# Performance work log

Hardware: AMD Instinct MI355X
Metric: run time of the kernel (lower is better)

Reference implementation:

```python
import jax, jax.numpy as jnp
import numpy as np
from jax import lax

# 4 directional difference kernels, stacked as OIHW [4,1,3,3]
# torch conv2d is cross-correlation; lax.conv_general_dilated with OIHW/NCHW matches.
_KERNELS = jnp.array([
    [[0, 0, 0], [-1, 1, 0], [0, 0, 0]],   # left:  x[i,j] - x[i,j-1]
    [[0, 0, 0], [0, 1, -1], [0, 0, 0]],   # right: x[i,j] - x[i,j+1]
    [[0, -1, 0], [0, 1, 0], [0, 0, 0]],   # up:    x[i,j] - x[i-1,j]
    [[0, 0, 0], [0, 1, 0], [0, -1, 0]],   # down:  x[i,j] - x[i+1,j]
], dtype=jnp.float32)[:, None, :, :]


def _avg_pool4(x):
    # x: [B,1,H,W] -> [B,1,H//4,W//4], non-overlapping 4x4 mean
    B, C, H, W = x.shape
    return x.reshape(B, C, H // 4, 4, W // 4, 4).mean(axis=(3, 5))


def _dir_diffs(x):
    # x: [B,1,h,w] -> [B,4,h,w]; zero-padded cross-correlation, padding=1
    return lax.conv_general_dilated(
        x, _KERNELS, window_strides=(1, 1), padding=((1, 1), (1, 1)),
        dimension_numbers=("NCHW", "OIHW", "NCHW"))


def setup_inputs() -> dict:
    key = jax.random.key(0)
    k1, k2 = jax.random.split(key)
    original = jax.random.uniform(k1, (32, 3, 512, 512), dtype=jnp.float32)
    enhanced = jax.random.uniform(k2, (32, 3, 512, 512), dtype=jnp.float32)
    return {"original": original, "enhanced": enhanced}


def reference(original, enhanced) -> jnp.ndarray:
    # channel mean, keepdim -> [B,1,H,W]
    o = jnp.mean(original, axis=1, keepdims=True)
    e = jnp.mean(enhanced, axis=1, keepdims=True)
    # 4x4 avg pool -> [B,1,H/4,W/4]
    op = _avg_pool4(o)
    ep = _avg_pool4(e)
    # 4 directional shift-diffs for both, squared differences summed over directions
    d = _dir_diffs(op) - _dir_diffs(ep)           # [B,4,h,w]
    loss = jnp.sum(d * d, axis=1, keepdims=True)  # [B,1,h,w]
    return loss
```

## Files before the change

### kernel.cpp

```cpp
#include <hip/hip_runtime.h>

#define HH 512
#define WW 512
#define PH 128
#define PW 128
#define CC 3

typedef float f32x4 __attribute__((ext_vector_type(4)));

__global__ void __launch_bounds__(256, 8)
pool_diff_kernel(const float* __restrict__ orig,
                 const float* __restrict__ enh,
                 float* __restrict__ g) {
    const int bid  = blockIdx.x;
    const int t    = threadIdx.x;
    const int half = t >> 7;
    const int pj   = t & 127;

    const int b    = bid >> 6;
    const int pr0  = (bid & 63) * 2;
    const int row0 = pr0 * 4;

    __shared__ float lds[2][256];

    float acc0 = 0.0f, acc1 = 0.0f;

    const size_t img     = (size_t)HH * WW;
    const size_t rowbase = (size_t)row0 * WW + (size_t)pj * 4;

#pragma unroll
    for (int s = 0; s < 6; ++s) {
        const float* src = (s < 3) ? orig : enh;
        const int    c   = (s < 3) ? s : s - 3;
        const float* p   = src + ((size_t)b * CC + c) * img + rowbase
                               + (size_t)half * WW;
        f32x4 v0 = *(const f32x4*)(p);
        f32x4 v1 = *(const f32x4*)(p + 2 * WW);
        f32x4 v2 = *(const f32x4*)(p + 4 * WW);
        f32x4 v3 = *(const f32x4*)(p + 6 * WW);
        const float s0 = (v0.x + v0.y) + (v0.z + v0.w);
        const float s1 = (v1.x + v1.y) + (v1.z + v1.w);
        const float s2 = (v2.x + v2.y) + (v2.z + v2.w);
        const float s3 = (v3.x + v3.y) + (v3.z + v3.w);
        if (s < 3) { acc0 += s0 + s1; acc1 += s2 + s3; }
        else       { acc0 -= s0 + s1; acc1 -= s2 + s3; }
        __syncthreads();
    }

    lds[0][t] = acc0;
    lds[1][t] = acc1;
    __syncthreads();

    if (t < 128) {
        const float v = (lds[0][t] + lds[0][t + 128]) * (1.0f / 48.0f);
        g[((size_t)b * PH + pr0) * PW + t] = v;
    } else {
        const int tj = t - 128;
        const float v = (lds[1][tj] + lds[1][t]) * (1.0f / 48.0f);
        g[((size_t)b * PH + (pr0 + 1)) * PW + tj] = v;
    }
}

__global__ void __launch_bounds__(256)
stencil_loss_kernel(const float* __restrict__ g,
                    float* __restrict__ out, int total) {
    int idx = blockIdx.x * blockDim.x + threadIdx.x;
    if (idx >= total) return;
    int j = idx & (PW - 1);
    int i = (idx >> 7) & (PH - 1);

    float c = g[idx];
    float l = (j > 0)      ? g[idx - 1]  : 0.0f;
    float r = (j < PW - 1) ? g[idx + 1]  : 0.0f;
    float u = (i > 0)      ? g[idx - PW] : 0.0f;
    float d = (i < PH - 1) ? g[idx + PW] : 0.0f;

    float dl = c - l, dr = c - r, du = c - u, dd = c - d;
    __builtin_nontemporal_store(dl * dl + dr * dr + du * du + dd * dd, out + idx);
}

extern "C" void kernel_launch(void* const* d_in, const int* in_sizes, int n_in,
                              void* d_out, int out_size, void* d_ws, size_t ws_size,
                              hipStream_t stream) {
    const float* orig = (const float*)d_in[0];
    const float* enh  = (const float*)d_in[1];
    float* out = (float*)d_out;
    float* g   = (float*)d_ws;

    const int batch = in_sizes[0] / (CC * HH * WW);
    const int total = batch * PH * PW;

    pool_diff_kernel<<<batch * 64, 256, 0, stream>>>(orig, enh, g);

    const int block = 256;
    const int grid = (total + block - 1) / block;
    stencil_loss_kernel<<<grid, block, 0, stream>>>(g, out, total);
}
```

Before: 210.7 us.

## Double-buffer channel loads via direct global-to-LDS async copies

Replaces the per-channel register loads in the pooling kernel with global_load_lds async copies into a double-buffered LDS tile. The next channel is prefetched while the current one is reduced, with explicit vmcnt waits and barriers. This aims to hide global memory latency in a bandwidth-bound reduction. In exchange it uses 32KB of LDS per block, which lowers occupancy, and drops the 8-waves occupancy hint.

```diff
diff --git a/kernel.cpp b/kernel.cpp
--- a/kernel.cpp
+++ b/kernel.cpp
@@ -8,12 +8,16 @@
 
 typedef float f32x4 __attribute__((ext_vector_type(4)));
 
-__global__ void __launch_bounds__(256, 8)
+__global__ void __launch_bounds__(256)
 pool_diff_kernel(const float* __restrict__ orig,
                  const float* __restrict__ enh,
                  float* __restrict__ g) {
+    __shared__ f32x4 buf[2][1024];
+
     const int bid  = blockIdx.x;
     const int t    = threadIdx.x;
+    const int wave = t >> 6;
+    const int lane = t & 63;
     const int half = t >> 7;
     const int pj   = t & 127;
 
@@ -21,43 +25,65 @@
     const int pr0  = (bid & 63) * 2;
     const int row0 = pr0 * 4;
 
-    __shared__ float lds[2][256];
+    const size_t img = (size_t)HH * WW;
+
+    auto stage = [&](int pb, int s2) {
+        const int    c    = (s2 < 3) ? s2 : s2 - 3;
+        const float* src  = (s2 < 3) ? orig : enh;
+        const float* base = src + ((size_t)b * CC + c) * img + (size_t)row0 * WW;
+        float*       lb   = (float*)&buf[pb][0];
+#pragma unroll
+        for (int q = 0; q < 4; ++q) {
+            const int unit = wave * 4 + q;
+            __builtin_amdgcn_global_load_lds(
+                (const __attribute__((address_space(1))) void*)(base + unit * 256 + lane * 4),
+                (__attribute__((address_space(3))) void*)(lb + unit * 256),
+                16, 0, 0);
+        }
+    };
 
     float acc0 = 0.0f, acc1 = 0.0f;
 
-    const size_t img     = (size_t)HH * WW;
-    const size_t rowbase = (size_t)row0 * WW + (size_t)pj * 4;
-
+    stage(0, 0);
 #pragma unroll
     for (int s = 0; s < 6; ++s) {
-        const float* src = (s < 3) ? orig : enh;
-        const int    c   = (s < 3) ? s : s - 3;
-        const float* p   = src + ((size_t)b * CC + c) * img + rowbase
-                               + (size_t)half * WW;
-        f32x4 v0 = *(const f32x4*)(p);
-        f32x4 v1 = *(const f32x4*)(p + 2 * WW);
-        f32x4 v2 = *(const f32x4*)(p + 4 * WW);
-        f32x4 v3 = *(const f32x4*)(p + 6 * WW);
-        const float s0 = (v0.x + v0.y) + (v0.z + v0.w);
-        const float s1 = (v1.x + v1.y) + (v1.z + v1.w);
-        const float s2 = (v2.x + v2.y) + (v2.z + v2.w);
-        const float s3 = (v3.x + v3.y) + (v3.z + v3.w);
-        if (s < 3) { acc0 += s0 + s1; acc1 += s2 + s3; }
-        else       { acc0 -= s0 + s1; acc1 -= s2 + s3; }
-        __syncthreads();
+        const int pb = s & 1;
+        if (s < 5) {
+            stage(pb ^ 1, s + 1);
+            asm volatile("s_waitcnt vmcnt(4)" ::: "memory");
+        } else {
+            asm volatile("s_waitcnt vmcnt(0)" ::: "memory");
+        }
+        __builtin_amdgcn_sched_barrier(0);
+        __builtin_amdgcn_s_barrier();
+        __builtin_amdgcn_sched_barrier(0);
+
+        const f32x4* B = &buf[pb][0];
+        f32x4 v0 = B[(0 + half) * 128 + pj];
+        f32x4 v1 = B[(2 + half) * 128 + pj];
+        f32x4 v2 = B[(4 + half) * 128 + pj];
+        f32x4 v3 = B[(6 + half) * 128 + pj];
+        const float s01 = ((v0.x + v0.y) + (v0.z + v0.w))
+                        + ((v1.x + v1.y) + (v1.z + v1.w));
+        const float s23 = ((v2.x + v2.y) + (v2.z + v2.w))
+                        + ((v3.x + v3.y) + (v3.z + v3.w));
+        if (s < 3) { acc0 += s01; acc1 += s23; }
+        else       { acc0 -= s01; acc1 -= s23; }
+
+        asm volatile("s_waitcnt lgkmcnt(0)" ::: "memory");
+        __builtin_amdgcn_sched_barrier(0);
+        __builtin_amdgcn_s_barrier();
     }
 
-    lds[0][t] = acc0;
-    lds[1][t] = acc1;
+    float* cb = (float*)&buf[0][0];
+    cb[t]       = acc0;
+    cb[256 + t] = acc1;
     __syncthreads();
-
     if (t < 128) {
-        const float v = (lds[0][t] + lds[0][t + 128]) * (1.0f / 48.0f);
-        g[((size_t)b * PH + pr0) * PW + t] = v;
+        g[((size_t)b * PH + pr0) * PW + t] = (cb[t] + cb[t + 128]) * (1.0f / 48.0f);
     } else {
         const int tj = t - 128;
-        const float v = (lds[1][tj] + lds[1][t]) * (1.0f / 48.0f);
-        g[((size_t)b * PH + (pr0 + 1)) * PW + tj] = v;
+        g[((size_t)b * PH + pr0 + 1) * PW + tj] = (cb[256 + tj] + cb[256 + t]) * (1.0f / 48.0f);
     }
 }
 
```

After: 212.4 us. Within noise of the previous version (+0.8%).
